# Kernel optimization log

Hardware: AMD Instinct MI355X
Metric: run time of the kernel (lower is better)

The kernel has to match this reference:

```python
import jax, jax.numpy as jnp
import numpy as np

NUM_EXPERTS = 16
TOP_K = 8
INIT_STD = 0.02

def setup_inputs() -> dict:
    key = jax.random.key(0)
    ks = jax.random.split(key, 5)
    B, S, H, I, E = 2, 2048, 2048, 768, NUM_EXPERTS
    return {
        "hidden_states": jax.random.normal(ks[0], (B, S, H), jnp.float32),
        "w_router": jax.random.normal(ks[1], (H, E), jnp.float32) * INIT_STD,
        "w_gate": jax.random.normal(ks[2], (E, H, I), jnp.float32) * INIT_STD,
        "w_up": jax.random.normal(ks[3], (E, H, I), jnp.float32) * INIT_STD,
        "w_down": jax.random.normal(ks[4], (E, I, H), jnp.float32) * INIT_STD,
    }

def reference(hidden_states, w_router, w_gate, w_up, w_down):
    # Router: logits -> fp32 softmax -> top-k -> renormalize (norm_topk_prob=True)
    router_logits = jnp.einsum("bsh,he->bse", hidden_states, w_router)  # [B,S,E]
    routing_weights = jax.nn.softmax(router_logits.astype(jnp.float32), axis=-1)
    topk_w, topk_idx = jax.lax.top_k(routing_weights, k=TOP_K)  # [B,S,K]
    topk_w = topk_w / topk_w.sum(axis=-1, keepdims=True)
    # Dense per-expert combine weights [B,S,E] (sum over top-k slots matching each expert)
    dense_w = jnp.sum(jax.nn.one_hot(topk_idx, NUM_EXPERTS, dtype=topk_w.dtype) * topk_w[..., None], axis=2)
    dense_w = dense_w.astype(hidden_states.dtype)
    # Every expert runs on all tokens (as in the source loop), vectorized over E
    gate = jax.nn.silu(jnp.einsum("bsh,ehi->besi", hidden_states, w_gate))  # [B,E,S,I]
    up = jnp.einsum("bsh,ehi->besi", hidden_states, w_up)
    expert_out = jnp.einsum("besi,eih->besh", gate * up, w_down)  # [B,E,S,H]
    final = jnp.einsum("bse,besh->bsh", dense_w, expert_out)
    return final, router_logits
```

## Files before the change

### kernel.cpp

```cpp
#include <hip/hip_runtime.h>
#include <hip/hip_bf16.h>


typedef __attribute__((ext_vector_type(8))) short short8;
typedef __attribute__((ext_vector_type(4))) float f32x4;

#define NUM_T 4096
#define DH    2048
#define DI    768
#define NE    16
#define DKD   (NE*DI)
#define MAXMT 20
#define HSC_CAP 2560
#define TOK_HALF 2048
#define FINAL_ELEMS ((size_t)NUM_T*DH)


static __device__ __forceinline__ unsigned short f2bf(float f) {
  unsigned int u = __builtin_bit_cast(unsigned int, f);
  u += 0x7fffu + ((u >> 16) & 1u);
  return (unsigned short)(u >> 16);
}

static __device__ __forceinline__ float bf2f(unsigned short b) {
  unsigned int u = ((unsigned int)b) << 16;
  return __builtin_bit_cast(float, u);
}

static __device__ __forceinline__ void gload16(const void* g, void* l) {
  __builtin_amdgcn_global_load_lds(
      (__attribute__((address_space(1))) void*)(g),
      (__attribute__((address_space(3))) void*)(l), 16, 0, 0);
}


__global__ __launch_bounds__(256)
void cvt_hidden_k(const float* __restrict__ in, unsigned short* __restrict__ out) {
  size_t i = (size_t)blockIdx.x * 256 + threadIdx.x;
  const float4* p = (const float4*)in + i * 2;
  float4 a = p[0], b = p[1];
  short8 v;
  v[0] = (short)f2bf(a.x); v[1] = (short)f2bf(a.y);
  v[2] = (short)f2bf(a.z); v[3] = (short)f2bf(a.w);
  v[4] = (short)f2bf(b.x); v[5] = (short)f2bf(b.y);
  v[6] = (short)f2bf(b.z); v[7] = (short)f2bf(b.w);
  *(short8*)(out + i * 8) = v;
}


__global__ __launch_bounds__(256)
void transpose_cvt_k(const float* __restrict__ in, unsigned short* __restrict__ out,
                     int R, int C, long inStrideE, long outStrideE, int outLD) {
  __shared__ float tile[32][33];
  const float* inE = in + (size_t)blockIdx.z * inStrideE;
  unsigned short* outE = out + (size_t)blockIdx.z * outStrideE;
  int c0 = blockIdx.x * 32, r0 = blockIdx.y * 32;
  int tx = threadIdx.x, ty = threadIdx.y;
#pragma unroll
  for (int i = 0; i < 4; i++)
    tile[ty * 4 + i][tx] = inE[(size_t)(r0 + ty * 4 + i) * C + c0 + tx];
  __syncthreads();
#pragma unroll
  for (int i = 0; i < 4; i++) {
    int c = ty * 4 + i;
    outE[(size_t)(c0 + c) * outLD + r0 + tx] = f2bf(tile[tx][c]);
  }
}


__global__ __launch_bounds__(256)
void router_k(const float* __restrict__ x, const float* __restrict__ wr,
              float* __restrict__ logits_out, unsigned short* __restrict__ dwb,
              unsigned char* __restrict__ slt) {
  int t = blockIdx.x;
  int tid = threadIdx.x, lane = tid & 63, wid = tid >> 6;
  float acc[16];
#pragma unroll
  for (int e = 0; e < 16; e++) acc[e] = 0.f;
  const float* xt = x + (size_t)t * DH;
  for (int i = tid; i < DH; i += 256) {
    float hv = xt[i];
    const float4* w4 = (const float4*)(wr + (size_t)i * 16);
#pragma unroll
    for (int q = 0; q < 4; q++) {
      float4 w = w4[q];
      acc[q * 4 + 0] += hv * w.x; acc[q * 4 + 1] += hv * w.y;
      acc[q * 4 + 2] += hv * w.z; acc[q * 4 + 3] += hv * w.w;
    }
  }
#pragma unroll
  for (int e = 0; e < 16; e++) {
#pragma unroll
    for (int off = 32; off; off >>= 1) acc[e] += __shfl_xor(acc[e], off, 64);
  }
  __shared__ float red[4][16];
  if (lane == 0) {
#pragma unroll
    for (int e = 0; e < 16; e++) red[wid][e] = acc[e];
  }
  __syncthreads();
  if (tid == 0) {
    float lg[16];
#pragma unroll
    for (int e = 0; e < 16; e++) lg[e] = red[0][e] + red[1][e] + red[2][e] + red[3][e];
    float mx = lg[0];
#pragma unroll
    for (int e = 1; e < 16; e++) mx = fmaxf(mx, lg[e]);
    float p[16], s = 0.f;
#pragma unroll
    for (int e = 0; e < 16; e++) { p[e] = __expf(lg[e] - mx); s += p[e]; }
    float inv = 1.f / s;
#pragma unroll
    for (int e = 0; e < 16; e++) p[e] *= inv;
    float tmp[16];
#pragma unroll
    for (int e = 0; e < 16; e++) tmp[e] = p[e];
    int idx[8]; float val[8]; float ts = 0.f;
#pragma unroll
    for (int k = 0; k < 8; k++) {
      int b = 0; float bv = tmp[0];
#pragma unroll
      for (int e = 1; e < 16; e++) { if (tmp[e] > bv) { bv = tmp[e]; b = e; } }
      idx[k] = b; val[k] = bv; tmp[b] = -1.f; ts += bv;
    }
    float dw[16];
    unsigned char sl[16];
#pragma unroll
    for (int e = 0; e < 16; e++) { dw[e] = 0.f; sl[e] = 0xFF; }
    float invt = 1.f / ts;
#pragma unroll
    for (int k = 0; k < 8; k++) { dw[idx[k]] += val[k] * invt; sl[idx[k]] = (unsigned char)k; }
#pragma unroll
    for (int e = 0; e < 16; e++) {
      dwb[(size_t)t * 16 + e] = f2bf(dw[e]);
      slt[(size_t)t * 16 + e] = sl[e];
      logits_out[(size_t)t * 16 + e] = lg[e];
    }
  }
}


__global__ __launch_bounds__(256)
void build_lists_k(const unsigned short* __restrict__ dwb,
                   const unsigned char* __restrict__ slt,
                   unsigned short* __restrict__ lst, int* __restrict__ meta) {
  int e = blockIdx.x;
  int tid = threadIdx.x;
  unsigned short loc[16]; int c = 0;
#pragma unroll
  for (int j = 0; j < 16; j++) {
    int t = tid * 16 + j;
    if (dwb[(size_t)t * 16 + e] != 0) {
      unsigned short s = slt[(size_t)t * 16 + e];
      loc[c++] = (unsigned short)(t | (s << 12));
    }
  }
  __shared__ int sc[256];
  __shared__ int pre[257];
  sc[tid] = c;
  __syncthreads();
  if (tid == 0) {
    int s = 0;
    for (int i = 0; i < 256; i++) { pre[i] = s; s += sc[i]; }
    pre[256] = s;
  }
  __syncthreads();
  unsigned short* L = lst + (size_t)e * NUM_T;
  int base = pre[tid];
  for (int j = 0; j < c; j++) L[base + j] = loc[j];
  int total = pre[256];
  for (int i = total + tid; i < NUM_T; i += 256) L[i] = 0xFFFFu;
  if (tid == 0) { meta[e * 2] = pre[128]; meta[e * 2 + 1] = total; }
}


__global__ __launch_bounds__(256, 3)
void gateup_k(const unsigned short* __restrict__ hbf,
              const unsigned short* __restrict__ wgbt,
              const unsigned short* __restrict__ wubt,
              const unsigned short* __restrict__ dwb,
              const unsigned short* __restrict__ lst,
              unsigned short* __restrict__ hsC) {
  const int bxr = blockIdx.x;
  const int wl  = (bxr & 7) * 480 + (bxr >> 3);
  const int e   = wl / 240;
  const int rem = wl - e * 240;
  const int n0  = (rem / MAXMT) * 64;
  const int m0  = (rem % MAXMT) * 128;

  const unsigned short* L = lst + (size_t)e * NUM_T;
  if (L[m0] & 0x8000) return;

  const int tid = threadIdx.x, lane = tid & 63, wid = tid >> 6;
  const int wm = wid >> 1, wn = wid & 1;
  const int lr = lane & 15, lgp = lane >> 4;

  __shared__ alignas(16) unsigned short As [3 * 128 * 32];
  __shared__ alignas(16) unsigned short Bgs[3 *  64 * 32];
  __shared__ alignas(16) unsigned short Bus[3 *  64 * 32];

  f32x4 zero = {0.f, 0.f, 0.f, 0.f};
  f32x4 accg[4][2], accu[4][2];
#pragma unroll
  for (int m = 0; m < 4; m++)
#pragma unroll
    for (int n = 0; n < 2; n++) { accg[m][n] = zero; accu[m][n] = zero; }

  const unsigned short* wgE = wgbt + (size_t)e * DI * DH;
  const unsigned short* wuE = wubt + (size_t)e * DI * DH;

  const int srow    = lane >> 2;
  const int schunk8 = (((lane & 3) - ((lane >> 3) & 3)) & 3) * 8;

  const int ar0 = m0 + wid * 32 + srow, ar1 = ar0 + 16;
  const unsigned short t0 = L[ar0], t1 = L[ar1];
  const size_t prow0 = (t0 & 0x8000) ? 0 : (size_t)(t0 & 0xFFF);
  const size_t prow1 = (t1 & 0x8000) ? 0 : (size_t)(t1 & 0xFFF);
  const size_t brow = (size_t)(n0 + wid * 16 + srow);

  const int slot8 = (((lane >> 4) + ((lane >> 1) & 3)) & 3) * 8;

  auto stage = [&](int b, int k0) {
    unsigned short* Ab = As  + b * 4096 + wid * 1024;
    unsigned short* Gb = Bgs + b * 2048 + wid * 512;
    unsigned short* Ub = Bus + b * 2048 + wid * 512;
    gload16(hbf + prow0 * DH + k0 + schunk8, Ab);
    gload16(hbf + prow1 * DH + k0 + schunk8, Ab + 512);
    gload16(wgE + brow  * DH + k0 + schunk8, Gb);
    gload16(wuE + brow  * DH + k0 + schunk8, Ub);
  };

  auto compute = [&](int b) {
    const unsigned short* Ab = As  + b * 4096;
    const unsigned short* Gb = Bgs + b * 2048;
    const unsigned short* Ub = Bus + b * 2048;
    short8 a[4], bg[2], bu[2];
#pragma unroll
    for (int m = 0; m < 4; m++)
      a[m] = *(const short8*)(Ab + (wm * 64 + m * 16 + lr) * 32 + slot8);
#pragma unroll
    for (int n = 0; n < 2; n++) {
      bg[n] = *(const short8*)(Gb + (wn * 32 + n * 16 + lr) * 32 + slot8);
      bu[n] = *(const short8*)(Ub + (wn * 32 + n * 16 + lr) * 32 + slot8);
    }
#pragma unroll
    for (int m = 0; m < 4; m++)
#pragma unroll
      for (int n = 0; n < 2; n++) {
        accg[m][n] = __builtin_amdgcn_mfma_f32_16x16x32_bf16(a[m], bg[n], accg[m][n], 0, 0, 0);
        accu[m][n] = __builtin_amdgcn_mfma_f32_16x16x32_bf16(a[m], bu[n], accu[m][n], 0, 0, 0);
      }
  };

  const int NT = DH / 32;
  stage(0, 0);
  stage(1, 32);
  int bc = 0, bs = 2;
#pragma unroll 1
  for (int i = 0; i < NT - 1; ++i) {
    asm volatile("s_waitcnt vmcnt(4)" ::: "memory");
    __builtin_amdgcn_s_barrier();
    __builtin_amdgcn_sched_barrier(0);
    compute(bc);
    if (i + 2 < NT) stage(bs, (i + 2) * 32);
    bc = (bc == 2) ? 0 : bc + 1;
    bs = (bs == 2) ? 0 : bs + 1;
  }
  asm volatile("s_waitcnt vmcnt(0)" ::: "memory");
  __builtin_amdgcn_s_barrier();
  __builtin_amdgcn_sched_barrier(0);
  compute(bc);

#pragma unroll
  for (int m = 0; m < 4; m++) {
#pragma unroll
    for (int r = 0; r < 4; r++) {
      int mrow = m0 + wm * 64 + m * 16 + 4 * lgp + r;
      unsigned short en = L[mrow];
      if (en & 0x8000) continue;
      int tp = en & 0xFFF;
      float w = bf2f(dwb[(size_t)tp * 16 + e]);
#pragma unroll
      for (int n = 0; n < 2; n++) {
        float g = accg[m][n][r], u = accu[m][n][r];
        float sig = 1.f / (1.f + __expf(-g));
        float val = g * sig * u * w;
        hsC[((size_t)e * HSC_CAP + mrow) * DI + n0 + wn * 32 + n * 16 + lr] = f2bf(val);
      }
    }
  }
}


__global__ __launch_bounds__(256, 3)
void down_half_k(const unsigned short* __restrict__ hsC,
                 const unsigned short* __restrict__ wdbt,
                 const unsigned short* __restrict__ lst,
                 const int* __restrict__ meta,
                 unsigned short* __restrict__ slotbuf, int hf) {
  const int bxr = blockIdx.x;
  const int wl  = (bxr & 7) * 320 + (bxr >> 3);
  const int e   = wl / 160;
  const int rem = wl - e * 160;
  const int n0  = (rem / 10) * 128;
  const int m0  = (rem % 10) * 128;

  const int rs = hf ? meta[e * 2] : 0;
  const int re = hf ? meta[e * 2 + 1] : meta[e * 2];
  const int rcount = re - rs;
  if (m0 >= rcount) return;

  const int tid = threadIdx.x, lane = tid & 63, wid = tid >> 6;
  const int wm = wid >> 1, wn = wid & 1;
  const int lr = lane & 15, lgp = lane >> 4;

  __shared__ alignas(16) unsigned short As[3 * 128 * 32];
  __shared__ alignas(16) unsigned short Bs[3 * 128 * 32];

  f32x4 zero = {0.f, 0.f, 0.f, 0.f};
  f32x4 acc[4][4];
#pragma unroll
  for (int m = 0; m < 4; m++)
#pragma unroll
    for (int n = 0; n < 4; n++) acc[m][n] = zero;

  const int srow    = lane >> 2;
  const int schunk8 = (((lane & 3) - ((lane >> 3) & 3)) & 3) * 8;
  const int sOff0   = wid * 1024;
  const int sOff1   = sOff0 + 512;
  const size_t arow0 = (size_t)(e * HSC_CAP + rs + m0 + wid * 32 + srow);
  const size_t arow1 = arow0 + 16;
  const size_t brow0 = (size_t)(n0 + wid * 32 + srow), brow1 = brow0 + 16;
  const int slot8 = (((lane >> 4) + ((lane >> 1) & 3)) & 3) * 8;

  const unsigned short* wdE = wdbt + (size_t)e * DI;

  auto stage = [&](int b, int k0) {
    unsigned short* Ab = As + b * 4096;
    unsigned short* Bb = Bs + b * 4096;
    gload16(hsC + arow0 * DI + k0 + schunk8, Ab + sOff0);
    gload16(hsC + arow1 * DI + k0 + schunk8, Ab + sOff1);
    gload16(wdE + brow0 * DKD + k0 + schunk8, Bb + sOff0);
    gload16(wdE + brow1 * DKD + k0 + schunk8, Bb + sOff1);
  };

  auto compute = [&](int bsel) {
    const unsigned short* Ab = As + bsel * 4096;
    const unsigned short* Bb = Bs + bsel * 4096;
    short8 a[4], b[4];
#pragma unroll
    for (int m = 0; m < 4; m++)
      a[m] = *(const short8*)(Ab + (size_t)(wm * 64 + m * 16 + lr) * 32 + slot8);
#pragma unroll
    for (int n = 0; n < 4; n++)
      b[n] = *(const short8*)(Bb + (size_t)(wn * 64 + n * 16 + lr) * 32 + slot8);
#pragma unroll
    for (int m = 0; m < 4; m++)
#pragma unroll
      for (int n = 0; n < 4; n++)
        acc[m][n] = __builtin_amdgcn_mfma_f32_16x16x32_bf16(a[m], b[n], acc[m][n], 0, 0, 0);
  };

  const int NT = DI / 32;
  stage(0, 0);
  stage(1, 32);
  int bc = 0, bs = 2;
#pragma unroll 1
  for (int i = 0; i < NT - 1; ++i) {
    asm volatile("s_waitcnt vmcnt(4)" ::: "memory");
    __builtin_amdgcn_s_barrier();
    __builtin_amdgcn_sched_barrier(0);
    compute(bc);
    if (i + 2 < NT) stage(bs, (i + 2) * 32);
    bc = (bc == 2) ? 0 : bc + 1;
    bs = (bs == 2) ? 0 : bs + 1;
  }
  asm volatile("s_waitcnt vmcnt(0)" ::: "memory");
  __builtin_amdgcn_s_barrier();
  __builtin_amdgcn_sched_barrier(0);
  compute(bc);

  const unsigned short* L = lst + (size_t)e * NUM_T;
#pragma unroll
  for (int m = 0; m < 4; m++) {
#pragma unroll
    for (int r = 0; r < 4; r++) {
      int gr = m0 + wm * 64 + m * 16 + 4 * lgp + r;
      if (gr >= rcount) continue;
      unsigned short en = L[rs + gr];
      int t  = en & 0xFFF;
      int s  = (en >> 12) & 7;
      int tl = t - hf * TOK_HALF;
#pragma unroll
      for (int n = 0; n < 4; n++)
        slotbuf[((size_t)s * TOK_HALF + tl) * DH + n0 + wn * 64 + n * 16 + lr] =
            f2bf(acc[m][n][r]);
    }
  }
}


__global__ __launch_bounds__(256)
void reduce_half_k(const unsigned short* __restrict__ slotbuf,
                   float* __restrict__ outp, int hf) {
  size_t i  = (size_t)blockIdx.x * 256 + threadIdx.x;
  size_t tl = i >> 8;
  size_t h0 = (i & 255) * 8;
  float sum[8];
#pragma unroll
  for (int j = 0; j < 8; j++) sum[j] = 0.f;
#pragma unroll
  for (int s = 0; s < 8; s++) {
    short8 v = *(const short8*)(slotbuf + ((size_t)s * TOK_HALF + tl) * DH + h0);
#pragma unroll
    for (int j = 0; j < 8; j++) sum[j] += bf2f((unsigned short)v[j]);
  }
  float* o = outp + ((size_t)(hf * TOK_HALF) + tl) * DH + h0;
  float4 o0 = {sum[0], sum[1], sum[2], sum[3]};
  float4 o1 = {sum[4], sum[5], sum[6], sum[7]};
  *(float4*)o = o0;
  *(float4*)(o + 4) = o1;
}


extern "C" void kernel_launch(void* const* d_in, const int* in_sizes, int n_in,
                              void* d_out, int out_size, void* d_ws, size_t ws_size,
                              hipStream_t stream) {
  const float* x  = (const float*)d_in[0];
  const float* wr = (const float*)d_in[1];
  const float* wg = (const float*)d_in[2];
  const float* wu = (const float*)d_in[3];
  const float* wd = (const float*)d_in[4];

  float* outF = (float*)d_out;
  float* outL = outF + FINAL_ELEMS;

  if (ws_size < 180682880ull) return;
  char* ws = (char*)d_ws;
  unsigned short* hbf   = (unsigned short*)(ws);
  unsigned short* wubt  = (unsigned short*)(ws + 16777216);
  unsigned short* hsC   = (unsigned short*)(ws + 67108864);
  unsigned short* wgbt  = (unsigned short*)(ws + 130023424);
  unsigned short* dwb   = (unsigned short*)(ws + 180355072);
  unsigned short* lst   = (unsigned short*)(ws + 180486144);
  unsigned char*  slt   = (unsigned char*) (ws + 180617216);
  int*            meta  = (int*)           (ws + 180682752);
  unsigned short* sbuf  = (unsigned short*)(ws);
  unsigned short* wdbt  = wgbt;

  cvt_hidden_k<<<4096, 256, 0, stream>>>(x, hbf);
  transpose_cvt_k<<<dim3(24, 64, 16), dim3(32, 8), 0, stream>>>(
      wg, wgbt, 2048, 768, (long)2048 * 768, (long)768 * 2048, 2048);
  transpose_cvt_k<<<dim3(24, 64, 16), dim3(32, 8), 0, stream>>>(
      wu, wubt, 2048, 768, (long)2048 * 768, (long)768 * 2048, 2048);
  router_k<<<4096, 256, 0, stream>>>(x, wr, outL, dwb, slt);
  build_lists_k<<<16, 256, 0, stream>>>(dwb, slt, lst, meta);
  gateup_k<<<3840, 256, 0, stream>>>(hbf, wgbt, wubt, dwb, lst, hsC);
  transpose_cvt_k<<<dim3(64, 24, 16), dim3(32, 8), 0, stream>>>(
      wd, wdbt, 768, 2048, (long)768 * 2048, 768L, 12288);
  down_half_k<<<2560, 256, 0, stream>>>(hsC, wdbt, lst, meta, sbuf, 0);
  reduce_half_k<<<2048, 256, 0, stream>>>(sbuf, outF, 0);
  down_half_k<<<2560, 256, 0, stream>>>(hsC, wdbt, lst, meta, sbuf, 1);
  reduce_half_k<<<2048, 256, 0, stream>>>(sbuf, outF, 1);
}
```

Baseline: 638.8 us.

## Interleave gate/up weights and enlarge gate-up GEMM tile to 256x128

Gate and up weights are transposed into one interleaved buffer with blocks of 64 gate rows followed by 64 up rows, so one B tile of 128 columns covers both. The gate-up kernel now uses 256x128 tiles with double-buffered B, triple-buffered A, and explicit LDS-read/MFMA interleaving with setprio. The up half is passed between waves through LDS in bf16 for the SwiGLU epilogue. This raises arithmetic intensity and halves the block count, at the cost of lower occupancy (launch bounds 2), more registers, and bf16 rounding of the up projection before the multiply.

```diff
diff --git a/kernel.cpp b/kernel.cpp
--- a/kernel.cpp
+++ b/kernel.cpp
@@ -10,9 +10,9 @@
 #define DI    768
 #define NE    16
 #define DKD   (NE*DI)
-#define MAXMT 20
 #define HSC_CAP 2560
 #define TOK_HALF 2048
+#define GU_NT (DH/32)
 #define FINAL_ELEMS ((size_t)NUM_T*DH)
 
 
@@ -50,7 +50,8 @@
 
 __global__ __launch_bounds__(256)
 void transpose_cvt_k(const float* __restrict__ in, unsigned short* __restrict__ out,
-                     int R, int C, long inStrideE, long outStrideE, int outLD) {
+                     int C, long inStrideE, long outStrideE, int outLD,
+                     int rShift, int rStrd, int rOff) {
   __shared__ float tile[32][33];
   const float* inE = in + (size_t)blockIdx.z * inStrideE;
   unsigned short* outE = out + (size_t)blockIdx.z * outStrideE;
@@ -63,7 +64,9 @@
 #pragma unroll
   for (int i = 0; i < 4; i++) {
     int c = ty * 4 + i;
-    outE[(size_t)(c0 + c) * outLD + r0 + tx] = f2bf(tile[tx][c]);
+    int r = c0 + c;
+    int s = ((r >> rShift) * rStrd) + rOff + (r & ((1 << rShift) - 1));
+    outE[(size_t)s * outLD + r0 + tx] = f2bf(tile[tx][c]);
   }
 }
 
@@ -174,118 +177,145 @@
 }
 
 
-__global__ __launch_bounds__(256, 3)
+__global__ __launch_bounds__(256, 2)
 void gateup_k(const unsigned short* __restrict__ hbf,
-              const unsigned short* __restrict__ wgbt,
-              const unsigned short* __restrict__ wubt,
+              const unsigned short* __restrict__ wgubt,
               const unsigned short* __restrict__ dwb,
               const unsigned short* __restrict__ lst,
               unsigned short* __restrict__ hsC) {
   const int bxr = blockIdx.x;
-  const int wl  = (bxr & 7) * 480 + (bxr >> 3);
-  const int e   = wl / 240;
-  const int rem = wl - e * 240;
-  const int n0  = (rem / MAXMT) * 64;
-  const int m0  = (rem % MAXMT) * 128;
+  const int wl  = (bxr & 7) * 240 + (bxr >> 3);
+  const int e   = wl / 120;
+  const int rem = wl - e * 120;
+  const int j   = rem / 10;
+  const int m0  = (rem % 10) * 256;
 
   const unsigned short* L = lst + (size_t)e * NUM_T;
   if (L[m0] & 0x8000) return;
 
   const int tid = threadIdx.x, lane = tid & 63, wid = tid >> 6;
-  const int wm = wid >> 1, wn = wid & 1;
+  const int wr = wid >> 1, wc = wid & 1;
   const int lr = lane & 15, lgp = lane >> 4;
 
-  __shared__ alignas(16) unsigned short As [3 * 128 * 32];
-  __shared__ alignas(16) unsigned short Bgs[3 *  64 * 32];
-  __shared__ alignas(16) unsigned short Bus[3 *  64 * 32];
+  __shared__ alignas(16) unsigned short ALDS[3 * 256 * 32];
+  __shared__ alignas(16) unsigned short BLDS[2 * 128 * 32];
 
   f32x4 zero = {0.f, 0.f, 0.f, 0.f};
-  f32x4 accg[4][2], accu[4][2];
-#pragma unroll
-  for (int m = 0; m < 4; m++)
-#pragma unroll
-    for (int n = 0; n < 2; n++) { accg[m][n] = zero; accu[m][n] = zero; }
-
-  const unsigned short* wgE = wgbt + (size_t)e * DI * DH;
-  const unsigned short* wuE = wubt + (size_t)e * DI * DH;
+  f32x4 acc[8][4];
+#pragma unroll
+  for (int m = 0; m < 8; m++)
+#pragma unroll
+    for (int n = 0; n < 4; n++) acc[m][n] = zero;
+
+  const unsigned short* wgubtE = wgubt + (size_t)e * 1536 * DH;
 
   const int srow    = lane >> 2;
   const int schunk8 = (((lane & 3) - ((lane >> 3) & 3)) & 3) * 8;
-
-  const int ar0 = m0 + wid * 32 + srow, ar1 = ar0 + 16;
-  const unsigned short t0 = L[ar0], t1 = L[ar1];
-  const size_t prow0 = (t0 & 0x8000) ? 0 : (size_t)(t0 & 0xFFF);
-  const size_t prow1 = (t1 & 0x8000) ? 0 : (size_t)(t1 & 0xFFF);
-  const size_t brow = (size_t)(n0 + wid * 16 + srow);
-
-  const int slot8 = (((lane >> 4) + ((lane >> 1) & 3)) & 3) * 8;
-
-  auto stage = [&](int b, int k0) {
-    unsigned short* Ab = As  + b * 4096 + wid * 1024;
-    unsigned short* Gb = Bgs + b * 2048 + wid * 512;
-    unsigned short* Ub = Bus + b * 2048 + wid * 512;
-    gload16(hbf + prow0 * DH + k0 + schunk8, Ab);
-    gload16(hbf + prow1 * DH + k0 + schunk8, Ab + 512);
-    gload16(wgE + brow  * DH + k0 + schunk8, Gb);
-    gload16(wuE + brow  * DH + k0 + schunk8, Ub);
-  };
-
-  auto compute = [&](int b) {
-    const unsigned short* Ab = As  + b * 4096;
-    const unsigned short* Gb = Bgs + b * 2048;
-    const unsigned short* Ub = Bus + b * 2048;
-    short8 a[4], bg[2], bu[2];
-#pragma unroll
-    for (int m = 0; m < 4; m++)
-      a[m] = *(const short8*)(Ab + (wm * 64 + m * 16 + lr) * 32 + slot8);
-#pragma unroll
-    for (int n = 0; n < 2; n++) {
-      bg[n] = *(const short8*)(Gb + (wn * 32 + n * 16 + lr) * 32 + slot8);
-      bu[n] = *(const short8*)(Ub + (wn * 32 + n * 16 + lr) * 32 + slot8);
-    }
-#pragma unroll
-    for (int m = 0; m < 4; m++)
-#pragma unroll
-      for (int n = 0; n < 2; n++) {
-        accg[m][n] = __builtin_amdgcn_mfma_f32_16x16x32_bf16(a[m], bg[n], accg[m][n], 0, 0, 0);
-        accu[m][n] = __builtin_amdgcn_mfma_f32_16x16x32_bf16(a[m], bu[n], accu[m][n], 0, 0, 0);
-      }
-  };
-
-  const int NT = DH / 32;
-  stage(0, 0);
-  stage(1, 32);
-  int bc = 0, bs = 2;
+  const int slot8   = (((lane >> 4) + ((lane >> 1) & 3)) & 3) * 8;
+
+  const unsigned short* gA[4];
+#pragma unroll
+  for (int i = 0; i < 4; i++) {
+    unsigned short en = L[m0 + wid * 64 + i * 16 + srow];
+    size_t tok = (en & 0x8000) ? 0 : (size_t)(en & 0xFFF);
+    gA[i] = hbf + tok * DH + schunk8;
+  }
+  const unsigned short* gB[2];
+#pragma unroll
+  for (int i = 0; i < 2; i++)
+    gB[i] = wgubtE + ((size_t)j * 128 + wid * 32 + i * 16 + srow) * DH + schunk8;
+
+#define STAGE_A(buf, t, i) gload16(gA[i] + (size_t)(t) * 32, \
+    ALDS + (buf) * 8192 + (wid * 64 + (i) * 16) * 32)
+#define STAGE_B(buf, t, i) gload16(gB[i] + (size_t)(t) * 32, \
+    BLDS + (buf) * 4096 + (wid * 32 + (i) * 16) * 32)
+#define RD_A(mf) (*(const short8*)(Ab + (wr * 128 + (mf) * 16 + lr) * 32 + slot8))
+#define RD_B(nf) (*(const short8*)(Bb + (wc * 64 + (nf) * 16 + lr) * 32 + slot8))
+#define MFMA4(m0_, m1_, m2_, m3_, n_) \
+    acc[m0_][n_] = __builtin_amdgcn_mfma_f32_16x16x32_bf16(a[m0_], b[n_], acc[m0_][n_], 0, 0, 0); \
+    acc[m1_][n_] = __builtin_amdgcn_mfma_f32_16x16x32_bf16(a[m1_], b[n_], acc[m1_][n_], 0, 0, 0); \
+    acc[m2_][n_] = __builtin_amdgcn_mfma_f32_16x16x32_bf16(a[m2_], b[n_], acc[m2_][n_], 0, 0, 0); \
+    acc[m3_][n_] = __builtin_amdgcn_mfma_f32_16x16x32_bf16(a[m3_], b[n_], acc[m3_][n_], 0, 0, 0);
+
+  STAGE_B(0, 0, 0); STAGE_B(0, 0, 1);
+  STAGE_A(0, 0, 0); STAGE_A(0, 0, 1); STAGE_A(0, 0, 2); STAGE_A(0, 0, 3);
+  STAGE_A(1, 1, 0); STAGE_A(1, 1, 1); STAGE_A(1, 1, 2); STAGE_A(1, 1, 3);
+
+  int ra = 0, rb = 0, sa = 2;
+  short8 a[8], b[4];
 #pragma unroll 1
-  for (int i = 0; i < NT - 1; ++i) {
-    asm volatile("s_waitcnt vmcnt(4)" ::: "memory");
+  for (int t = 0; t < GU_NT; ++t) {
+    if (t < GU_NT - 1) asm volatile("s_waitcnt vmcnt(4)" ::: "memory");
+    else               asm volatile("s_waitcnt vmcnt(0)" ::: "memory");
     __builtin_amdgcn_s_barrier();
     __builtin_amdgcn_sched_barrier(0);
-    compute(bc);
-    if (i + 2 < NT) stage(bs, (i + 2) * 32);
-    bc = (bc == 2) ? 0 : bc + 1;
-    bs = (bs == 2) ? 0 : bs + 1;
-  }
-  asm volatile("s_waitcnt vmcnt(0)" ::: "memory");
-  __builtin_amdgcn_s_barrier();
-  __builtin_amdgcn_sched_barrier(0);
-  compute(bc);
-
-#pragma unroll
-  for (int m = 0; m < 4; m++) {
-#pragma unroll
-    for (int r = 0; r < 4; r++) {
-      int mrow = m0 + wm * 64 + m * 16 + 4 * lgp + r;
-      unsigned short en = L[mrow];
-      if (en & 0x8000) continue;
-      int tp = en & 0xFFF;
-      float w = bf2f(dwb[(size_t)tp * 16 + e]);
-#pragma unroll
-      for (int n = 0; n < 2; n++) {
-        float g = accg[m][n][r], u = accu[m][n][r];
-        float sig = 1.f / (1.f + __expf(-g));
-        float val = g * sig * u * w;
-        hsC[((size_t)e * HSC_CAP + mrow) * DI + n0 + wn * 32 + n * 16 + lr] = f2bf(val);
+    const unsigned short* Ab = ALDS + ra * 8192;
+    const unsigned short* Bb = BLDS + rb * 4096;
+    if (t + 1 < GU_NT) { STAGE_B(rb ^ 1, t + 1, 0); STAGE_B(rb ^ 1, t + 1, 1); }
+    a[0] = RD_A(0); a[1] = RD_A(1); a[2] = RD_A(2); a[3] = RD_A(3);
+    b[0] = RD_B(0); b[1] = RD_B(1);
+    asm volatile("s_waitcnt lgkmcnt(0)" ::: "memory");
+    __builtin_amdgcn_sched_barrier(0);
+    __builtin_amdgcn_s_setprio(1);
+    MFMA4(0, 1, 2, 3, 0); MFMA4(0, 1, 2, 3, 1);
+    __builtin_amdgcn_s_setprio(0);
+    if (t + 2 < GU_NT) { STAGE_A(sa, t + 2, 0); STAGE_A(sa, t + 2, 1); }
+    a[4] = RD_A(4); a[5] = RD_A(5); a[6] = RD_A(6); a[7] = RD_A(7);
+    asm volatile("s_waitcnt lgkmcnt(0)" ::: "memory");
+    __builtin_amdgcn_sched_barrier(0);
+    __builtin_amdgcn_s_setprio(1);
+    MFMA4(4, 5, 6, 7, 0); MFMA4(4, 5, 6, 7, 1);
+    __builtin_amdgcn_s_setprio(0);
+    if (t + 2 < GU_NT) { STAGE_A(sa, t + 2, 2); STAGE_A(sa, t + 2, 3); }
+    b[2] = RD_B(2); b[3] = RD_B(3);
+    asm volatile("s_waitcnt lgkmcnt(0)" ::: "memory");
+    __builtin_amdgcn_sched_barrier(0);
+    __builtin_amdgcn_s_setprio(1);
+    MFMA4(4, 5, 6, 7, 2); MFMA4(4, 5, 6, 7, 3);
+    __builtin_amdgcn_s_setprio(0);
+    __builtin_amdgcn_s_setprio(1);
+    MFMA4(0, 1, 2, 3, 2); MFMA4(0, 1, 2, 3, 3);
+    __builtin_amdgcn_s_setprio(0);
+    ra = (ra == 2) ? 0 : ra + 1;
+    sa = (sa == 2) ? 0 : sa + 1;
+    rb ^= 1;
+  }
+#undef STAGE_A
+#undef STAGE_B
+#undef RD_A
+#undef RD_B
+#undef MFMA4
+
+  __syncthreads();
+  unsigned short (*exch)[64] = (unsigned short(*)[64])ALDS;
+  if (wc == 1) {
+#pragma unroll
+    for (int mf = 0; mf < 8; mf++)
+#pragma unroll
+      for (int nf = 0; nf < 4; nf++)
+#pragma unroll
+        for (int r = 0; r < 4; r++)
+          exch[wr * 128 + mf * 16 + lgp * 4 + r][nf * 16 + lr] = f2bf(acc[mf][nf][r]);
+  }
+  __syncthreads();
+  if (wc == 0) {
+#pragma unroll
+    for (int mf = 0; mf < 8; mf++) {
+#pragma unroll
+      for (int r = 0; r < 4; r++) {
+        int m = wr * 128 + mf * 16 + lgp * 4 + r;
+        unsigned short en = L[m0 + m];
+        if (en & 0x8000) continue;
+        int tp = en & 0xFFF;
+        float w = bf2f(dwb[(size_t)tp * 16 + e]);
+#pragma unroll
+        for (int nf = 0; nf < 4; nf++) {
+          float g = acc[mf][nf][r];
+          float u = bf2f(exch[m][nf * 16 + lr]);
+          float sig = 1.f / (1.f + __expf(-g));
+          hsC[((size_t)e * HSC_CAP + m0 + m) * DI + j * 64 + nf * 16 + lr]
+              = f2bf(sig * g * u * w);
+        }
       }
     }
   }
@@ -438,26 +468,25 @@
   if (ws_size < 180682880ull) return;
   char* ws = (char*)d_ws;
   unsigned short* hbf   = (unsigned short*)(ws);
-  unsigned short* wubt  = (unsigned short*)(ws + 16777216);
-  unsigned short* hsC   = (unsigned short*)(ws + 67108864);
-  unsigned short* wgbt  = (unsigned short*)(ws + 130023424);
+  unsigned short* wgubt = (unsigned short*)(ws + 16777216);
+  unsigned short* hsC   = (unsigned short*)(ws + 117440512);
   unsigned short* dwb   = (unsigned short*)(ws + 180355072);
   unsigned short* lst   = (unsigned short*)(ws + 180486144);
   unsigned char*  slt   = (unsigned char*) (ws + 180617216);
   int*            meta  = (int*)           (ws + 180682752);
   unsigned short* sbuf  = (unsigned short*)(ws);
-  unsigned short* wdbt  = wgbt;
+  unsigned short* wdbt  = (unsigned short*)(ws + 67108864);
 
   cvt_hidden_k<<<4096, 256, 0, stream>>>(x, hbf);
   transpose_cvt_k<<<dim3(24, 64, 16), dim3(32, 8), 0, stream>>>(
-      wg, wgbt, 2048, 768, (long)2048 * 768, (long)768 * 2048, 2048);
+      wg, wgubt, 768, (long)2048 * 768, (long)1536 * 2048, 2048, 6, 128, 0);
   transpose_cvt_k<<<dim3(24, 64, 16), dim3(32, 8), 0, stream>>>(
-      wu, wubt, 2048, 768, (long)2048 * 768, (long)768 * 2048, 2048);
+      wu, wgubt, 768, (long)2048 * 768, (long)1536 * 2048, 2048, 6, 128, 64);
   router_k<<<4096, 256, 0, stream>>>(x, wr, outL, dwb, slt);
   build_lists_k<<<16, 256, 0, stream>>>(dwb, slt, lst, meta);
-  gateup_k<<<3840, 256, 0, stream>>>(hbf, wgbt, wubt, dwb, lst, hsC);
+  gateup_k<<<1920, 256, 0, stream>>>(hbf, wgubt, dwb, lst, hsC);
   transpose_cvt_k<<<dim3(64, 24, 16), dim3(32, 8), 0, stream>>>(
-      wd, wdbt, 768, 2048, (long)768 * 2048, 768L, 12288);
+      wd, wdbt, 2048, (long)768 * 2048, 768L, 12288, 11, 2048, 0);
   down_half_k<<<2560, 256, 0, stream>>>(hsC, wdbt, lst, meta, sbuf, 0);
   reduce_half_k<<<2048, 256, 0, stream>>>(sbuf, outF, 0);
   down_half_k<<<2560, 256, 0, stream>>>(hsC, wdbt, lst, meta, sbuf, 1);
```

Result: slower. 721.5 us (+13.0%).

## Load gate/up A operand directly into registers and widen transpose kernel tiles

Applied to the files above, without the earlier changes.

The gate/up GEMM no longer stages the gathered hidden-state rows through shared memory. Each wave loads its A fragments straight from global memory into registers, double-buffered one tile ahead, while B tiles stay in LDS with a triple buffer, and MFMA blocks run at raised priority. The transpose-convert kernel now handles 128x32 tiles with 4-wide bf16 stores, and gate and up weights are converted in one merged launch. This cuts LDS traffic and kernel launch count, at the cost of uncoalesced, redundant global reads of A across waves and more registers.

```diff
diff --git a/kernel.cpp b/kernel.cpp
--- a/kernel.cpp
+++ b/kernel.cpp
@@ -4,6 +4,7 @@
 
 typedef __attribute__((ext_vector_type(8))) short short8;
 typedef __attribute__((ext_vector_type(4))) float f32x4;
+typedef __attribute__((ext_vector_type(4))) unsigned short us4;
 
 #define NUM_T 4096
 #define DH    2048
@@ -49,21 +50,28 @@
 
 
 __global__ __launch_bounds__(256)
-void transpose_cvt_k(const float* __restrict__ in, unsigned short* __restrict__ out,
-                     int R, int C, long inStrideE, long outStrideE, int outLD) {
-  __shared__ float tile[32][33];
-  const float* inE = in + (size_t)blockIdx.z * inStrideE;
-  unsigned short* outE = out + (size_t)blockIdx.z * outStrideE;
-  int c0 = blockIdx.x * 32, r0 = blockIdx.y * 32;
-  int tx = threadIdx.x, ty = threadIdx.y;
-#pragma unroll
-  for (int i = 0; i < 4; i++)
-    tile[ty * 4 + i][tx] = inE[(size_t)(r0 + ty * 4 + i) * C + c0 + tx];
+void transpose_cvt_k(const float* __restrict__ s0, unsigned short* __restrict__ d0,
+                     const float* __restrict__ s1, unsigned short* __restrict__ d1,
+                     int C, long inStrideE, long outStrideE, int outLD) {
+  __shared__ float tile[128][33];
+  const int zz = blockIdx.z, e = zz & 15;
+  const float* inE = (zz < 16 ? s0 : s1) + (size_t)e * inStrideE;
+  unsigned short* outE = (zz < 16 ? d0 : d1) + (size_t)e * outStrideE;
+  const int r0 = blockIdx.x * 128, c0 = blockIdx.y * 32;
+  const int tid = threadIdx.x;
+  const int lc = tid & 31, rg = tid >> 5;
+#pragma unroll
+  for (int i = 0; i < 16; i++)
+    tile[rg * 16 + i][lc] = inE[(size_t)(r0 + rg * 16 + i) * C + c0 + lc];
   __syncthreads();
+  const int u = tid & 31, cg = tid >> 5;
 #pragma unroll
   for (int i = 0; i < 4; i++) {
-    int c = ty * 4 + i;
-    outE[(size_t)(c0 + c) * outLD + r0 + tx] = f2bf(tile[tx][c]);
+    int c = cg * 4 + i;
+    us4 v;
+    v[0] = f2bf(tile[u * 4 + 0][c]); v[1] = f2bf(tile[u * 4 + 1][c]);
+    v[2] = f2bf(tile[u * 4 + 2][c]); v[3] = f2bf(tile[u * 4 + 3][c]);
+    *(us4*)(outE + (size_t)(c0 + c) * outLD + r0 + u * 4) = v;
   }
 }
 
@@ -195,9 +203,8 @@
   const int wm = wid >> 1, wn = wid & 1;
   const int lr = lane & 15, lgp = lane >> 4;
 
-  __shared__ alignas(16) unsigned short As [3 * 128 * 32];
-  __shared__ alignas(16) unsigned short Bgs[3 *  64 * 32];
-  __shared__ alignas(16) unsigned short Bus[3 *  64 * 32];
+  __shared__ alignas(16) unsigned short Bgs[3 * 64 * 32];
+  __shared__ alignas(16) unsigned short Bus[3 * 64 * 32];
 
   f32x4 zero = {0.f, 0.f, 0.f, 0.f};
   f32x4 accg[4][2], accu[4][2];
@@ -211,78 +218,85 @@
 
   const int srow    = lane >> 2;
   const int schunk8 = (((lane & 3) - ((lane >> 3) & 3)) & 3) * 8;
-
-  const int ar0 = m0 + wid * 32 + srow, ar1 = ar0 + 16;
-  const unsigned short t0 = L[ar0], t1 = L[ar1];
-  const size_t prow0 = (t0 & 0x8000) ? 0 : (size_t)(t0 & 0xFFF);
-  const size_t prow1 = (t1 & 0x8000) ? 0 : (size_t)(t1 & 0xFFF);
+  const int slot8   = (((lane >> 4) + ((lane >> 1) & 3)) & 3) * 8;
+
   const size_t brow = (size_t)(n0 + wid * 16 + srow);
-
-  const int slot8 = (((lane >> 4) + ((lane >> 1) & 3)) & 3) * 8;
-
-  auto stage = [&](int b, int k0) {
-    unsigned short* Ab = As  + b * 4096 + wid * 1024;
-    unsigned short* Gb = Bgs + b * 2048 + wid * 512;
-    unsigned short* Ub = Bus + b * 2048 + wid * 512;
-    gload16(hbf + prow0 * DH + k0 + schunk8, Ab);
-    gload16(hbf + prow1 * DH + k0 + schunk8, Ab + 512);
-    gload16(wgE + brow  * DH + k0 + schunk8, Gb);
-    gload16(wuE + brow  * DH + k0 + schunk8, Ub);
-  };
-
-  auto compute = [&](int b) {
-    const unsigned short* Ab = As  + b * 4096;
-    const unsigned short* Gb = Bgs + b * 2048;
-    const unsigned short* Ub = Bus + b * 2048;
-    short8 a[4], bg[2], bu[2];
-#pragma unroll
-    for (int m = 0; m < 4; m++)
-      a[m] = *(const short8*)(Ab + (wm * 64 + m * 16 + lr) * 32 + slot8);
-#pragma unroll
-    for (int n = 0; n < 2; n++) {
-      bg[n] = *(const short8*)(Gb + (wn * 32 + n * 16 + lr) * 32 + slot8);
-      bu[n] = *(const short8*)(Ub + (wn * 32 + n * 16 + lr) * 32 + slot8);
-    }
-#pragma unroll
-    for (int m = 0; m < 4; m++)
-#pragma unroll
-      for (int n = 0; n < 2; n++) {
-        accg[m][n] = __builtin_amdgcn_mfma_f32_16x16x32_bf16(a[m], bg[n], accg[m][n], 0, 0, 0);
-        accu[m][n] = __builtin_amdgcn_mfma_f32_16x16x32_bf16(a[m], bu[n], accu[m][n], 0, 0, 0);
-      }
-  };
-
-  const int NT = DH / 32;
-  stage(0, 0);
-  stage(1, 32);
-  int bc = 0, bs = 2;
+  const unsigned short* gG = wgE + brow * DH + schunk8;
+  const unsigned short* gU = wuE + brow * DH + schunk8;
+
+  const unsigned short* gA[4];
+#pragma unroll
+  for (int mf = 0; mf < 4; mf++) {
+    unsigned short en = L[m0 + wm * 64 + mf * 16 + lr];
+    gA[mf] = hbf + (size_t)((en & 0x8000) ? 0 : (en & 0xFFF)) * DH + lgp * 8;
+  }
+
+  short8 aA[4], aB[4], bg[2], bu[2];
+  int rb = 0, sb = 2;
+
+#define STB(buf, t) \
+    gload16(gG + (size_t)(t) * 32, Bgs + (buf) * 2048 + wid * 512); \
+    gload16(gU + (size_t)(t) * 32, Bus + (buf) * 2048 + wid * 512);
+#define LDA(dst, t) \
+    dst[0] = *(const short8*)(gA[0] + (size_t)(t) * 32); \
+    dst[1] = *(const short8*)(gA[1] + (size_t)(t) * 32); \
+    dst[2] = *(const short8*)(gA[2] + (size_t)(t) * 32); \
+    dst[3] = *(const short8*)(gA[3] + (size_t)(t) * 32);
+#define TILE_BODY(aUse, aLoad, t, DO_A, DO_B, WAIT) \
+    asm volatile("s_waitcnt vmcnt(" WAIT ")" ::: "memory"); \
+    __builtin_amdgcn_s_barrier(); \
+    __builtin_amdgcn_sched_barrier(0); \
+    if (DO_A) { LDA(aLoad, (t) + 1) } \
+    { const unsigned short* Gb = Bgs + rb * 2048; \
+      const unsigned short* Ub = Bus + rb * 2048; \
+      bg[0] = *(const short8*)(Gb + (wn * 32 + lr) * 32 + slot8); \
+      bg[1] = *(const short8*)(Gb + (wn * 32 + 16 + lr) * 32 + slot8); \
+      bu[0] = *(const short8*)(Ub + (wn * 32 + lr) * 32 + slot8); \
+      bu[1] = *(const short8*)(Ub + (wn * 32 + 16 + lr) * 32 + slot8); } \
+    if (DO_B) { STB(sb, (t) + 2) } \
+    asm volatile("s_waitcnt lgkmcnt(0)" ::: "memory"); \
+    __builtin_amdgcn_sched_barrier(0); \
+    __builtin_amdgcn_s_setprio(1); \
+    _Pragma("unroll") \
+    for (int m = 0; m < 4; m++) { \
+      accg[m][0] = __builtin_amdgcn_mfma_f32_16x16x32_bf16(aUse[m], bg[0], accg[m][0], 0, 0, 0); \
+      accg[m][1] = __builtin_amdgcn_mfma_f32_16x16x32_bf16(aUse[m], bg[1], accg[m][1], 0, 0, 0); \
+      accu[m][0] = __builtin_amdgcn_mfma_f32_16x16x32_bf16(aUse[m], bu[0], accu[m][0], 0, 0, 0); \
+      accu[m][1] = __builtin_amdgcn_mfma_f32_16x16x32_bf16(aUse[m], bu[1], accu[m][1], 0, 0, 0); \
+    } \
+    __builtin_amdgcn_s_setprio(0); \
+    rb = (rb == 2) ? 0 : rb + 1; \
+    sb = (sb == 2) ? 0 : sb + 1;
+
+  LDA(aA, 0)
+  STB(0, 0)
+  STB(1, 1)
+
 #pragma unroll 1
-  for (int i = 0; i < NT - 1; ++i) {
-    asm volatile("s_waitcnt vmcnt(4)" ::: "memory");
-    __builtin_amdgcn_s_barrier();
-    __builtin_amdgcn_sched_barrier(0);
-    compute(bc);
-    if (i + 2 < NT) stage(bs, (i + 2) * 32);
-    bc = (bc == 2) ? 0 : bc + 1;
-    bs = (bs == 2) ? 0 : bs + 1;
-  }
-  asm volatile("s_waitcnt vmcnt(0)" ::: "memory");
-  __builtin_amdgcn_s_barrier();
-  __builtin_amdgcn_sched_barrier(0);
-  compute(bc);
-
-#pragma unroll
-  for (int m = 0; m < 4; m++) {
+  for (int t2 = 0; t2 < 31; ++t2) {
+    const int t = t2 * 2;
+    TILE_BODY(aA, aB, t,     1, 1, "2")
+    TILE_BODY(aB, aA, t + 1, 1, 1, "2")
+  }
+  TILE_BODY(aA, aB, 62, 1, 0, "2")
+  TILE_BODY(aB, aA, 63, 0, 0, "0")
+
+#undef STB
+#undef LDA
+#undef TILE_BODY
+
+#pragma unroll
+  for (int mf = 0; mf < 4; mf++) {
 #pragma unroll
     for (int r = 0; r < 4; r++) {
-      int mrow = m0 + wm * 64 + m * 16 + 4 * lgp + r;
+      int mrow = m0 + wm * 64 + mf * 16 + 4 * lgp + r;
       unsigned short en = L[mrow];
       if (en & 0x8000) continue;
       int tp = en & 0xFFF;
       float w = bf2f(dwb[(size_t)tp * 16 + e]);
 #pragma unroll
       for (int n = 0; n < 2; n++) {
-        float g = accg[m][n][r], u = accu[m][n][r];
+        float g = accg[mf][n][r], u = accu[mf][n][r];
         float sig = 1.f / (1.f + __expf(-g));
         float val = g * sig * u * w;
         hsC[((size_t)e * HSC_CAP + mrow) * DI + n0 + wn * 32 + n * 16 + lr] = f2bf(val);
@@ -449,15 +463,13 @@
   unsigned short* wdbt  = wgbt;
 
   cvt_hidden_k<<<4096, 256, 0, stream>>>(x, hbf);
-  transpose_cvt_k<<<dim3(24, 64, 16), dim3(32, 8), 0, stream>>>(
-      wg, wgbt, 2048, 768, (long)2048 * 768, (long)768 * 2048, 2048);
-  transpose_cvt_k<<<dim3(24, 64, 16), dim3(32, 8), 0, stream>>>(
-      wu, wubt, 2048, 768, (long)2048 * 768, (long)768 * 2048, 2048);
+  transpose_cvt_k<<<dim3(16, 24, 32), 256, 0, stream>>>(
+      wg, wgbt, wu, wubt, 768, (long)2048 * 768, (long)768 * 2048, 2048);
   router_k<<<4096, 256, 0, stream>>>(x, wr, outL, dwb, slt);
   build_lists_k<<<16, 256, 0, stream>>>(dwb, slt, lst, meta);
   gateup_k<<<3840, 256, 0, stream>>>(hbf, wgbt, wubt, dwb, lst, hsC);
-  transpose_cvt_k<<<dim3(64, 24, 16), dim3(32, 8), 0, stream>>>(
-      wd, wdbt, 768, 2048, (long)768 * 2048, 768L, 12288);
+  transpose_cvt_k<<<dim3(6, 64, 16), 256, 0, stream>>>(
+      wd, wdbt, wd, wdbt, 2048, (long)768 * 2048, 768L, 12288);
   down_half_k<<<2560, 256, 0, stream>>>(hsC, wdbt, lst, meta, sbuf, 0);
   reduce_half_k<<<2048, 256, 0, stream>>>(sbuf, outF, 0);
   down_half_k<<<2560, 256, 0, stream>>>(hsC, wdbt, lst, meta, sbuf, 1);
```

After: 867.4 us. +35.8%, slower.

## Fuse hidden bf16 conversion into router and merge gate/up weight transposes

Applied to the files above, without the earlier changes.

Removes the separate hidden-state conversion kernel by having the router write the bf16 copy while it reads each token row. It merges the gate and up weight transpose-convert launches into one launch using a z-index selector. It also widens transpose tiles to 128 rows so each thread writes 4 bf16 values as a vector. This cuts launches and redundant reads of the input, at the cost of more shared memory per block and a different tile shape.

```diff
diff --git a/kernel.cpp b/kernel.cpp
--- a/kernel.cpp
+++ b/kernel.cpp
@@ -4,6 +4,7 @@
 
 typedef __attribute__((ext_vector_type(8))) short short8;
 typedef __attribute__((ext_vector_type(4))) float f32x4;
+typedef __attribute__((ext_vector_type(4))) unsigned short us4;
 
 #define NUM_T 4096
 #define DH    2048
@@ -35,35 +36,28 @@
 
 
 __global__ __launch_bounds__(256)
-void cvt_hidden_k(const float* __restrict__ in, unsigned short* __restrict__ out) {
-  size_t i = (size_t)blockIdx.x * 256 + threadIdx.x;
-  const float4* p = (const float4*)in + i * 2;
-  float4 a = p[0], b = p[1];
-  short8 v;
-  v[0] = (short)f2bf(a.x); v[1] = (short)f2bf(a.y);
-  v[2] = (short)f2bf(a.z); v[3] = (short)f2bf(a.w);
-  v[4] = (short)f2bf(b.x); v[5] = (short)f2bf(b.y);
-  v[6] = (short)f2bf(b.z); v[7] = (short)f2bf(b.w);
-  *(short8*)(out + i * 8) = v;
-}
-
-
-__global__ __launch_bounds__(256)
-void transpose_cvt_k(const float* __restrict__ in, unsigned short* __restrict__ out,
-                     int R, int C, long inStrideE, long outStrideE, int outLD) {
-  __shared__ float tile[32][33];
-  const float* inE = in + (size_t)blockIdx.z * inStrideE;
-  unsigned short* outE = out + (size_t)blockIdx.z * outStrideE;
-  int c0 = blockIdx.x * 32, r0 = blockIdx.y * 32;
-  int tx = threadIdx.x, ty = threadIdx.y;
-#pragma unroll
-  for (int i = 0; i < 4; i++)
-    tile[ty * 4 + i][tx] = inE[(size_t)(r0 + ty * 4 + i) * C + c0 + tx];
+void transpose_cvt_k(const float* __restrict__ s0, unsigned short* __restrict__ d0,
+                     const float* __restrict__ s1, unsigned short* __restrict__ d1,
+                     int C, long inStrideE, long outStrideE, int outLD) {
+  __shared__ float tile[128][33];
+  const int zz = blockIdx.z, e = zz & 15;
+  const float* inE = (zz < 16 ? s0 : s1) + (size_t)e * inStrideE;
+  unsigned short* outE = (zz < 16 ? d0 : d1) + (size_t)e * outStrideE;
+  const int r0 = blockIdx.x * 128, c0 = blockIdx.y * 32;
+  const int tid = threadIdx.x;
+  const int lc = tid & 31, rg = tid >> 5;
+#pragma unroll
+  for (int i = 0; i < 16; i++)
+    tile[rg * 16 + i][lc] = inE[(size_t)(r0 + rg * 16 + i) * C + c0 + lc];
   __syncthreads();
+  const int u = tid & 31, cg = tid >> 5;
 #pragma unroll
   for (int i = 0; i < 4; i++) {
-    int c = ty * 4 + i;
-    outE[(size_t)(c0 + c) * outLD + r0 + tx] = f2bf(tile[tx][c]);
+    int c = cg * 4 + i;
+    us4 v;
+    v[0] = f2bf(tile[u * 4 + 0][c]); v[1] = f2bf(tile[u * 4 + 1][c]);
+    v[2] = f2bf(tile[u * 4 + 2][c]); v[3] = f2bf(tile[u * 4 + 3][c]);
+    *(us4*)(outE + (size_t)(c0 + c) * outLD + r0 + u * 4) = v;
   }
 }
 
@@ -71,16 +65,26 @@
 __global__ __launch_bounds__(256)
 void router_k(const float* __restrict__ x, const float* __restrict__ wr,
               float* __restrict__ logits_out, unsigned short* __restrict__ dwb,
-              unsigned char* __restrict__ slt) {
+              unsigned char* __restrict__ slt, unsigned short* __restrict__ hbf) {
   int t = blockIdx.x;
   int tid = threadIdx.x, lane = tid & 63, wid = tid >> 6;
+  const float* xt = x + (size_t)t * DH;
+
+  const float4* p = (const float4*)(xt + tid * 8);
+  float4 va = p[0], vb = p[1];
+  float h[8] = {va.x, va.y, va.z, va.w, vb.x, vb.y, vb.z, vb.w};
+  short8 hv8;
+#pragma unroll
+  for (int j = 0; j < 8; j++) hv8[j] = (short)f2bf(h[j]);
+  *(short8*)(hbf + (size_t)t * DH + tid * 8) = hv8;
+
   float acc[16];
 #pragma unroll
   for (int e = 0; e < 16; e++) acc[e] = 0.f;
-  const float* xt = x + (size_t)t * DH;
-  for (int i = tid; i < DH; i += 256) {
-    float hv = xt[i];
-    const float4* w4 = (const float4*)(wr + (size_t)i * 16);
+#pragma unroll
+  for (int j = 0; j < 8; j++) {
+    const float4* w4 = (const float4*)(wr + (size_t)(tid * 8 + j) * 16);
+    float hv = h[j];
 #pragma unroll
     for (int q = 0; q < 4; q++) {
       float4 w = w4[q];
@@ -106,15 +110,15 @@
     float mx = lg[0];
 #pragma unroll
     for (int e = 1; e < 16; e++) mx = fmaxf(mx, lg[e]);
-    float p[16], s = 0.f;
-#pragma unroll
-    for (int e = 0; e < 16; e++) { p[e] = __expf(lg[e] - mx); s += p[e]; }
+    float p2[16], s = 0.f;
+#pragma unroll
+    for (int e = 0; e < 16; e++) { p2[e] = __expf(lg[e] - mx); s += p2[e]; }
     float inv = 1.f / s;
 #pragma unroll
-    for (int e = 0; e < 16; e++) p[e] *= inv;
+    for (int e = 0; e < 16; e++) p2[e] *= inv;
     float tmp[16];
 #pragma unroll
-    for (int e = 0; e < 16; e++) tmp[e] = p[e];
+    for (int e = 0; e < 16; e++) tmp[e] = p2[e];
     int idx[8]; float val[8]; float ts = 0.f;
 #pragma unroll
     for (int k = 0; k < 8; k++) {
@@ -448,16 +452,13 @@
   unsigned short* sbuf  = (unsigned short*)(ws);
   unsigned short* wdbt  = wgbt;
 
-  cvt_hidden_k<<<4096, 256, 0, stream>>>(x, hbf);
-  transpose_cvt_k<<<dim3(24, 64, 16), dim3(32, 8), 0, stream>>>(
-      wg, wgbt, 2048, 768, (long)2048 * 768, (long)768 * 2048, 2048);
-  transpose_cvt_k<<<dim3(24, 64, 16), dim3(32, 8), 0, stream>>>(
-      wu, wubt, 2048, 768, (long)2048 * 768, (long)768 * 2048, 2048);
-  router_k<<<4096, 256, 0, stream>>>(x, wr, outL, dwb, slt);
+  router_k<<<4096, 256, 0, stream>>>(x, wr, outL, dwb, slt, hbf);
   build_lists_k<<<16, 256, 0, stream>>>(dwb, slt, lst, meta);
+  transpose_cvt_k<<<dim3(16, 24, 32), 256, 0, stream>>>(
+      wg, wgbt, wu, wubt, 768, (long)2048 * 768, (long)768 * 2048, 2048);
   gateup_k<<<3840, 256, 0, stream>>>(hbf, wgbt, wubt, dwb, lst, hsC);
-  transpose_cvt_k<<<dim3(64, 24, 16), dim3(32, 8), 0, stream>>>(
-      wd, wdbt, 768, 2048, (long)768 * 2048, 768L, 12288);
+  transpose_cvt_k<<<dim3(6, 64, 16), 256, 0, stream>>>(
+      wd, wdbt, wd, wdbt, 2048, (long)768 * 2048, 768L, 12288);
   down_half_k<<<2560, 256, 0, stream>>>(hsC, wdbt, lst, meta, sbuf, 0);
   reduce_half_k<<<2048, 256, 0, stream>>>(sbuf, outF, 0);
   down_half_k<<<2560, 256, 0, stream>>>(hsC, wdbt, lst, meta, sbuf, 1);
```

New measurement: 669.9 us. +4.9%, slower.
